# Optimization experiments

Measured on AMD Instinct MI355X. Metric: run time of the kernel, lower is better.

## Reference

```python
import jax, jax.numpy as jnp
import numpy as np

ROUTER_AUX_LOSS_COEF = 0.001


def setup_inputs() -> dict:
    key = jax.random.key(0)
    k1, k2, k3, k4 = jax.random.split(key, 4)
    B, S, H = 2, 2048, 2048
    E, I = 8, 768
    return {
        "hidden_states": jax.random.normal(k1, (B, S, H), dtype=jnp.float32),
        "gate_w": jax.random.normal(k2, (H, E), dtype=jnp.float32) * 0.02,
        "gate_up_proj": jax.random.normal(k3, (E, 2 * I, H), dtype=jnp.float32) * 0.02,
        "down_proj": jax.random.normal(k4, (E, H, I), dtype=jnp.float32) * 0.02,
        "num_experts_per_tok": 2,
    }


def reference(hidden_states, gate_w, gate_up_proj, down_proj, num_experts_per_tok):
    B, S, H = hidden_states.shape
    E = gate_w.shape[1]
    x = hidden_states.reshape(-1, H)  # (T, H)
    T = x.shape[0]

    # Router
    router_logits = x @ gate_w  # (T, E)
    routing_weights = jax.nn.softmax(router_logits, axis=-1)
    topk_w, selected = jax.lax.top_k(routing_weights, num_experts_per_tok)  # (T, K)
    topk_w = topk_w / jnp.sum(topk_w, axis=-1, keepdims=True)  # norm_topk_prob

    # Dense (T, E) combine weights: zero for non-selected experts. Identical math
    # to gathering per-token expert weights, but avoids materializing (T,K,2I,H).
    w_dense = jnp.zeros((T, E), x.dtype).at[jnp.arange(T)[:, None], selected].set(topk_w)

    # Expert GEMMs over all experts (non-selected contributions get weight 0)
    gate_up = jnp.einsum("th,efh->tef", x, gate_up_proj)  # (T, E, 2I)
    gate, up = jnp.split(gate_up, 2, axis=-1)
    inter = jax.nn.silu(gate) * up  # (T, E, I)
    expert_out = jnp.einsum("tei,ehi->teh", inter, down_proj)  # (T, E, H)
    final = jnp.einsum("teh,te->th", expert_out, w_dense).reshape(B, S, H)

    # Load-balancing auxiliary loss
    expert_probs = jnp.mean(routing_weights, axis=0)  # (E,)
    expert_mask = jax.nn.one_hot(selected, E, dtype=x.dtype)  # (T, K, E)
    expert_freq = jnp.mean(jnp.sum(expert_mask, axis=1), axis=0)  # (E,)
    aux_loss = jnp.sum(expert_probs * expert_freq) * E * ROUTER_AUX_LOSS_COEF

    return final, router_logits, aux_loss
```

## Files before the change

### kernel.cpp

```cpp
#include <hip/hip_runtime.h>
#include <hip/hip_bf16.h>
#include <math.h>

#define TT 4096
#define HH 2048
#define EE 8
#define II 768
#define TWOI 1536

typedef __attribute__((ext_vector_type(8))) short bf16v8;
typedef __attribute__((ext_vector_type(4))) float f32x4;

static __device__ __forceinline__ void cvt8f(const float4 v0, const float4 v1,
                                             uint4& hi, uint4& lo) {
    unsigned u[8] = {__float_as_uint(v0.x), __float_as_uint(v0.y),
                     __float_as_uint(v0.z), __float_as_uint(v0.w),
                     __float_as_uint(v1.x), __float_as_uint(v1.y),
                     __float_as_uint(v1.z), __float_as_uint(v1.w)};
    unsigned s[8];
#pragma unroll
    for (int i = 0; i < 8; ++i) {
        const float r = __uint_as_float(u[i]) - __uint_as_float(u[i] & 0xFFFF0000u);
        s[i] = __float_as_uint(r);
    }
    hi.x = __builtin_amdgcn_perm(u[1], u[0], 0x07060302);
    hi.y = __builtin_amdgcn_perm(u[3], u[2], 0x07060302);
    hi.z = __builtin_amdgcn_perm(u[5], u[4], 0x07060302);
    hi.w = __builtin_amdgcn_perm(u[7], u[6], 0x07060302);
    lo.x = __builtin_amdgcn_perm(s[1], s[0], 0x07060302);
    lo.y = __builtin_amdgcn_perm(s[3], s[2], 0x07060302);
    lo.z = __builtin_amdgcn_perm(s[5], s[4], 0x07060302);
    lo.w = __builtin_amdgcn_perm(s[7], s[6], 0x07060302);
}

__global__ __launch_bounds__(256) void router_kernel(
    const float* __restrict__ x, const float* __restrict__ gw,
    float* __restrict__ logits_out, int* __restrict__ counts,
    int* __restrict__ bucket_tok, float* __restrict__ bucket_w)
{
    const int wave = threadIdx.x >> 6;
    const int lane = threadIdx.x & 63;
    const int t = blockIdx.x * 4 + wave;

    float acc[EE];
#pragma unroll
    for (int e = 0; e < EE; ++e) acc[e] = 0.f;

    const float4* xr = (const float4*)(x + (size_t)t * HH);
    for (int i = lane; i < HH / 4; i += 64) {
        const float4 v = xr[i];
        const float* g = gw + (size_t)(i * 4) * EE;
#pragma unroll
        for (int e = 0; e < EE; ++e)
            acc[e] += v.x * g[e] + v.y * g[e + EE]
                    + v.z * g[e + 2 * EE] + v.w * g[e + 3 * EE];
    }
#pragma unroll
    for (int e = 0; e < EE; ++e) {
#pragma unroll
        for (int off = 32; off > 0; off >>= 1)
            acc[e] += __shfl_xor(acc[e], off, 64);
    }

    if (lane == 0) {
        float mx = acc[0];
#pragma unroll
        for (int e = 1; e < EE; ++e) mx = fmaxf(mx, acc[e]);
        float p[EE]; float s = 0.f;
#pragma unroll
        for (int e = 0; e < EE; ++e) { p[e] = expf(acc[e] - mx); s += p[e]; }
        const float inv = 1.f / s;
#pragma unroll
        for (int e = 0; e < EE; ++e) {
            p[e] *= inv;
            logits_out[(size_t)t * EE + e] = acc[e];
        }
        int i0 = 0;
#pragma unroll
        for (int e = 1; e < EE; ++e) if (p[e] > p[i0]) i0 = e;
        int i1 = (i0 == 0) ? 1 : 0;
#pragma unroll
        for (int e = 0; e < EE; ++e) if (e != i0 && p[e] > p[i1]) i1 = e;
        const float denom = 1.f / (p[i0] + p[i1]);
        const float w0 = p[i0] * denom, w1 = p[i1] * denom;
        int pos0 = atomicAdd(&counts[i0], 1);
        bucket_tok[i0 * TT + pos0] = t; bucket_w[i0 * TT + pos0] = w0;
        int pos1 = atomicAdd(&counts[i1], 1);
        bucket_tok[i1 * TT + pos1] = t; bucket_w[i1 * TT + pos1] = w1;
    }
}

__global__ __launch_bounds__(256) void finalize_router(
    const float* __restrict__ logits, const int* __restrict__ counts,
    int* __restrict__ offsets, float* __restrict__ aux_out)
{
    __shared__ float sums[EE];
    if (threadIdx.x < EE) sums[threadIdx.x] = 0.f;
    __syncthreads();
    float loc[EE];
#pragma unroll
    for (int e = 0; e < EE; ++e) loc[e] = 0.f;
    for (int t = threadIdx.x; t < TT; t += 256) {
        const float* lr = logits + (size_t)t * EE;
        float l[EE]; float mx = -1e30f;
#pragma unroll
        for (int e = 0; e < EE; ++e) { l[e] = lr[e]; mx = fmaxf(mx, l[e]); }
        float s = 0.f, p[EE];
#pragma unroll
        for (int e = 0; e < EE; ++e) { p[e] = expf(l[e] - mx); s += p[e]; }
        const float inv = 1.f / s;
#pragma unroll
        for (int e = 0; e < EE; ++e) loc[e] += p[e] * inv;
    }
#pragma unroll
    for (int e = 0; e < EE; ++e) atomicAdd(&sums[e], loc[e]);
    __syncthreads();
    if (threadIdx.x == 0) {
        int o = 0; float aux = 0.f;
        for (int e = 0; e < EE; ++e) {
            offsets[e] = o; o += counts[e];
            aux += (sums[e] / (float)TT) * ((float)counts[e] / (float)TT);
        }
        aux_out[0] = aux * (float)EE * 0.001f;
    }
}

#define AHI 0
#define ALO 10240
#define BHI 20480
#define BLO 30720
#define LROW 80

__global__ __launch_bounds__(256, 2) void moe_gateup_v3(
    const float* __restrict__ x, const float* __restrict__ Wgu,
    const int* __restrict__ counts, const int* __restrict__ offsets,
    const int* __restrict__ bucket_tok, float* __restrict__ inter)
{
    const int bid = blockIdx.x;
    const int e = bid & 7;
    const int rem = bid >> 3;
    const int mb = rem / 12, nb = rem % 12;

    const int cnt = counts[e];
    const int m0 = mb * 128;
    if (m0 >= cnt) return;
    const int n0 = nb * 64;
    const int base = offsets[e];

    __shared__ unsigned char smem[40960];

    const int tid = threadIdx.x;
    const int lane = tid & 63;
    const int wid = tid >> 6;
    const int wm = wid >> 1, wn = wid & 1;

    const int srow = tid >> 1;
    const int sseg = tid & 1;
    const int arow = m0 + srow;
    const int atok = (arow < cnt) ? bucket_tok[e * TT + arow] : 0;
    const float* ag = x + (size_t)atok * HH + sseg * 16;
    const int bblk = srow >> 5, bc = srow & 31;
    const int bj = ((bblk & 1) ? II : 0) + n0 + ((bblk >> 1) << 5) + bc;
    const float* bg = Wgu + ((size_t)e * TWOI + bj) * HH + sseg * 16;
    const int au0 = srow * LROW + (sseg * 2 + 0) * 16;
    const int au1 = srow * LROW + (sseg * 2 + 1) * 16;

    int aoff[4], boff[4];
#pragma unroll
    for (int i = 0; i < 4; ++i) {
        const int ra = wm * 64 + i * 16 + (lane & 15);
        aoff[i] = ra * LROW + (lane >> 4) * 16;
        const int rb = wn * 64 + i * 16 + (lane & 15);
        boff[i] = rb * LROW + (lane >> 4) * 16;
    }

    f32x4 acc[4][4];
#pragma unroll
    for (int i = 0; i < 4; ++i)
#pragma unroll
        for (int j = 0; j < 4; ++j) acc[i][j] = f32x4{0.f, 0.f, 0.f, 0.f};

    float4 pa0 = *(const float4*)(ag + 0), pa1 = *(const float4*)(ag + 4);
    float4 pa2 = *(const float4*)(ag + 8), pa3 = *(const float4*)(ag + 12);
    float4 pb0 = *(const float4*)(bg + 0), pb1 = *(const float4*)(bg + 4);
    float4 pb2 = *(const float4*)(bg + 8), pb3 = *(const float4*)(bg + 12);

    const int NS = HH / 32;
    for (int s = 0; s < NS; ++s) {
        __syncthreads();
        uint4 hi, lo;
        cvt8f(pa0, pa1, hi, lo);
        *(uint4*)(smem + AHI + au0) = hi; *(uint4*)(smem + ALO + au0) = lo;
        cvt8f(pa2, pa3, hi, lo);
        *(uint4*)(smem + AHI + au1) = hi; *(uint4*)(smem + ALO + au1) = lo;
        cvt8f(pb0, pb1, hi, lo);
        *(uint4*)(smem + BHI + au0) = hi; *(uint4*)(smem + BLO + au0) = lo;
        cvt8f(pb2, pb3, hi, lo);
        *(uint4*)(smem + BHI + au1) = hi; *(uint4*)(smem + BLO + au1) = lo;
        __syncthreads();
        if (s + 1 < NS) {
            const int k0 = (s + 1) * 32;
            pa0 = *(const float4*)(ag + k0); pa1 = *(const float4*)(ag + k0 + 4);
            pa2 = *(const float4*)(ag + k0 + 8); pa3 = *(const float4*)(ag + k0 + 12);
            pb0 = *(const float4*)(bg + k0); pb1 = *(const float4*)(bg + k0 + 4);
            pb2 = *(const float4*)(bg + k0 + 8); pb3 = *(const float4*)(bg + k0 + 12);
        }
        bf16v8 ah[4], al[4], bh[4], bl[4];
#pragma unroll
        for (int i = 0; i < 4; ++i) {
            ah[i] = *(const bf16v8*)(smem + AHI + aoff[i]);
            al[i] = *(const bf16v8*)(smem + ALO + aoff[i]);
            bh[i] = *(const bf16v8*)(smem + BHI + boff[i]);
            bl[i] = *(const bf16v8*)(smem + BLO + boff[i]);
        }
#pragma unroll
        for (int i = 0; i < 4; ++i)
#pragma unroll
            for (int j = 0; j < 4; ++j) {
                acc[i][j] = __builtin_amdgcn_mfma_f32_16x16x32_bf16(ah[i], bh[j], acc[i][j], 0, 0, 0);
                acc[i][j] = __builtin_amdgcn_mfma_f32_16x16x32_bf16(ah[i], bl[j], acc[i][j], 0, 0, 0);
                acc[i][j] = __builtin_amdgcn_mfma_f32_16x16x32_bf16(al[i], bh[j], acc[i][j], 0, 0, 0);
            }
    }

#pragma unroll
    for (int mi = 0; mi < 4; ++mi)
#pragma unroll
        for (int np = 0; np < 2; ++np) {
            const f32x4 g = acc[mi][np], u = acc[mi][np + 2];
            const int colp = n0 + wn * 32 + np * 16 + (lane & 15);
#pragma unroll
            for (int j = 0; j < 4; ++j) {
                const int r = m0 + wm * 64 + mi * 16 + ((lane >> 4) << 2) + j;
                if (r < cnt) {
                    const float gg = g[j];
                    const float sv = gg / (1.f + expf(-gg));
                    inter[(size_t)(base + r) * II + colp] = sv * u[j];
                }
            }
        }
}

__global__ __launch_bounds__(256, 2) void moe_down_v3(
    const float* __restrict__ inter, const float* __restrict__ Wd,
    const int* __restrict__ counts, const int* __restrict__ offsets,
    const int* __restrict__ bucket_tok, const float* __restrict__ bucket_w,
    float* __restrict__ out)
{
    const int bid = blockIdx.x;
    const int e = bid & 7;
    const int rem = bid >> 3;
    const int mb = rem >> 4, nb = rem & 15;

    const int cnt = counts[e];
    const int m0 = mb * 128;
    if (m0 >= cnt) return;
    const int n0 = nb * 128;
    const int base = offsets[e];

    __shared__ unsigned char smem[40960];

    const int tid = threadIdx.x;
    const int lane = tid & 63;
    const int wid = tid >> 6;
    const int wm = wid >> 1, wn = wid & 1;

    const int srow = tid >> 1;
    const int sseg = tid & 1;
    const int arow = m0 + srow;
    const int asafe = (arow < cnt) ? arow : 0;
    const float* ag = inter + (size_t)(base + asafe) * II + sseg * 16;
    const float* bg = Wd + ((size_t)e * HH + n0 + srow) * II + sseg * 16;
    const int au0 = srow * LROW + (sseg * 2 + 0) * 16;
    const int au1 = srow * LROW + (sseg * 2 + 1) * 16;

    int aoff[4], boff[4];
#pragma unroll
    for (int i = 0; i < 4; ++i) {
        const int ra = wm * 64 + i * 16 + (lane & 15);
        aoff[i] = ra * LROW + (lane >> 4) * 16;
        const int rb = wn * 64 + i * 16 + (lane & 15);
        boff[i] = rb * LROW + (lane >> 4) * 16;
    }

    f32x4 acc[4][4];
#pragma unroll
    for (int i = 0; i < 4; ++i)
#pragma unroll
        for (int j = 0; j < 4; ++j) acc[i][j] = f32x4{0.f, 0.f, 0.f, 0.f};

    float4 pa0 = *(const float4*)(ag + 0), pa1 = *(const float4*)(ag + 4);
    float4 pa2 = *(const float4*)(ag + 8), pa3 = *(const float4*)(ag + 12);
    float4 pb0 = *(const float4*)(bg + 0), pb1 = *(const float4*)(bg + 4);
    float4 pb2 = *(const float4*)(bg + 8), pb3 = *(const float4*)(bg + 12);

    const int NS = II / 32;
    for (int s = 0; s < NS; ++s) {
        __syncthreads();
        uint4 hi, lo;
        cvt8f(pa0, pa1, hi, lo);
        *(uint4*)(smem + AHI + au0) = hi; *(uint4*)(smem + ALO + au0) = lo;
        cvt8f(pa2, pa3, hi, lo);
        *(uint4*)(smem + AHI + au1) = hi; *(uint4*)(smem + ALO + au1) = lo;
        cvt8f(pb0, pb1, hi, lo);
        *(uint4*)(smem + BHI + au0) = hi; *(uint4*)(smem + BLO + au0) = lo;
        cvt8f(pb2, pb3, hi, lo);
        *(uint4*)(smem + BHI + au1) = hi; *(uint4*)(smem + BLO + au1) = lo;
        __syncthreads();
        if (s + 1 < NS) {
            const int k0 = (s + 1) * 32;
            pa0 = *(const float4*)(ag + k0); pa1 = *(const float4*)(ag + k0 + 4);
            pa2 = *(const float4*)(ag + k0 + 8); pa3 = *(const float4*)(ag + k0 + 12);
            pb0 = *(const float4*)(bg + k0); pb1 = *(const float4*)(bg + k0 + 4);
            pb2 = *(const float4*)(bg + k0 + 8); pb3 = *(const float4*)(bg + k0 + 12);
        }
        bf16v8 ah[4], al[4], bh[4], bl[4];
#pragma unroll
        for (int i = 0; i < 4; ++i) {
            ah[i] = *(const bf16v8*)(smem + AHI + aoff[i]);
            al[i] = *(const bf16v8*)(smem + ALO + aoff[i]);
            bh[i] = *(const bf16v8*)(smem + BHI + boff[i]);
            bl[i] = *(const bf16v8*)(smem + BLO + boff[i]);
        }
#pragma unroll
        for (int i = 0; i < 4; ++i)
#pragma unroll
            for (int j = 0; j < 4; ++j) {
                acc[i][j] = __builtin_amdgcn_mfma_f32_16x16x32_bf16(ah[i], bh[j], acc[i][j], 0, 0, 0);
                acc[i][j] = __builtin_amdgcn_mfma_f32_16x16x32_bf16(ah[i], bl[j], acc[i][j], 0, 0, 0);
                acc[i][j] = __builtin_amdgcn_mfma_f32_16x16x32_bf16(al[i], bh[j], acc[i][j], 0, 0, 0);
            }
    }

#pragma unroll
    for (int mi = 0; mi < 4; ++mi) {
        int rtok[4]; float rw[4]; int rok[4];
#pragma unroll
        for (int j = 0; j < 4; ++j) {
            const int r = m0 + wm * 64 + mi * 16 + ((lane >> 4) << 2) + j;
            rok[j] = (r < cnt);
            rtok[j] = rok[j] ? bucket_tok[e * TT + r] : 0;
            rw[j] = rok[j] ? bucket_w[e * TT + r] : 0.f;
        }
#pragma unroll
        for (int ni = 0; ni < 4; ++ni) {
            const int col = n0 + wn * 64 + ni * 16 + (lane & 15);
#pragma unroll
            for (int j = 0; j < 4; ++j)
                if (rok[j])
                    atomicAdd(out + (size_t)rtok[j] * HH + col, rw[j] * acc[mi][ni][j]);
        }
    }
}

extern "C" void kernel_launch(void* const* d_in, const int* in_sizes, int n_in,
                              void* d_out, int out_size, void* d_ws, size_t ws_size,
                              hipStream_t stream)
{
    const float* x   = (const float*)d_in[0];
    const float* gw  = (const float*)d_in[1];
    const float* wgu = (const float*)d_in[2];
    const float* wd  = (const float*)d_in[3];

    float* out_final  = (float*)d_out;
    float* out_logits = out_final + (size_t)TT * HH;
    float* out_aux    = out_logits + (size_t)TT * EE;

    int*   counts     = (int*)d_ws;
    int*   offsets    = counts + 8;
    int*   bucket_tok = (int*)d_ws + 64;
    float* bucket_w   = (float*)d_ws + 64 + EE * TT;
    float* inter      = (float*)d_ws + 64 + 2 * EE * TT;

    hipMemsetAsync(d_ws, 0, 256, stream);
    hipMemsetAsync(d_out, 0, sizeof(float) * (size_t)TT * HH, stream);

    router_kernel<<<TT / 4, 256, 0, stream>>>(x, gw, out_logits, counts,
                                              bucket_tok, bucket_w);
    finalize_router<<<1, 256, 0, stream>>>(out_logits, counts, offsets, out_aux);
    moe_gateup_v3<<<12 * 32 * EE, 256, 0, stream>>>(x, wgu, counts, offsets,
                                                    bucket_tok, inter);
    moe_down_v3<<<16 * 32 * EE, 256, 0, stream>>>(inter, wd, counts, offsets,
                                                  bucket_tok, bucket_w, out_final);
}
```

Before: 647.5 us.

## Enlarge expert GEMM tiles to 128x256 with per-wave full-M layout

Both expert GEMM kernels switch from 128x128 tiles on a 2x2 wave grid to wider tiles (N doubled). Each wave now covers all 128 rows and a 64-column slice, so B fragments stay in registers and A fragments are streamed from shared memory. The goal is to cut global loads and the fp32-to-bf16 split conversion of A per FLOP, and to halve the block count. The cost is a larger shared memory footprint (60KB) and doubled accumulator registers (128 floats), which may lower occupancy or cause spills under launch_bounds(256,2).

```diff
diff --git a/kernel.cpp b/kernel.cpp
--- a/kernel.cpp
+++ b/kernel.cpp
@@ -128,10 +128,10 @@
 #define AHI 0
 #define ALO 10240
 #define BHI 20480
-#define BLO 30720
+#define BLO 40960
 #define LROW 80
 
-__global__ __launch_bounds__(256, 2) void moe_gateup_v3(
+__global__ __launch_bounds__(256, 2) void moe_gateup_v4(
     const float* __restrict__ x, const float* __restrict__ Wgu,
     const int* __restrict__ counts, const int* __restrict__ offsets,
     const int* __restrict__ bucket_tok, float* __restrict__ inter)
@@ -139,51 +139,67 @@
     const int bid = blockIdx.x;
     const int e = bid & 7;
     const int rem = bid >> 3;
-    const int mb = rem / 12, nb = rem % 12;
+    const int mb = rem / 6, nb = rem % 6;
 
     const int cnt = counts[e];
     const int m0 = mb * 128;
     if (m0 >= cnt) return;
-    const int n0 = nb * 64;
+    const int n0 = nb * 128;
     const int base = offsets[e];
 
-    __shared__ unsigned char smem[40960];
+    __shared__ unsigned char smem[61440];
 
     const int tid = threadIdx.x;
     const int lane = tid & 63;
-    const int wid = tid >> 6;
-    const int wm = wid >> 1, wn = wid & 1;
+    const int w = tid >> 6;
 
     const int srow = tid >> 1;
     const int sseg = tid & 1;
     const int arow = m0 + srow;
     const int atok = (arow < cnt) ? bucket_tok[e * TT + arow] : 0;
     const float* ag = x + (size_t)atok * HH + sseg * 16;
-    const int bblk = srow >> 5, bc = srow & 31;
-    const int bj = ((bblk & 1) ? II : 0) + n0 + ((bblk >> 1) << 5) + bc;
-    const float* bg = Wgu + ((size_t)e * TWOI + bj) * HH + sseg * 16;
+
+    int bcol[2];
+#pragma unroll
+    for (int h = 0; h < 2; ++h) {
+        const int r = srow + h * 128;
+        const int wq = r >> 6, sub = r & 63;
+        bcol[h] = ((sub >> 5) ? II : 0) + n0 + wq * 32 + (sub & 31);
+    }
+    const float* bg0 = Wgu + ((size_t)e * TWOI + bcol[0]) * HH + sseg * 16;
+    const float* bg1 = Wgu + ((size_t)e * TWOI + bcol[1]) * HH + sseg * 16;
+
     const int au0 = srow * LROW + (sseg * 2 + 0) * 16;
     const int au1 = srow * LROW + (sseg * 2 + 1) * 16;
-
-    int aoff[4], boff[4];
-#pragma unroll
-    for (int i = 0; i < 4; ++i) {
-        const int ra = wm * 64 + i * 16 + (lane & 15);
+    const int bu0 = srow * LROW + (sseg * 2 + 0) * 16;
+    const int bu1 = srow * LROW + (sseg * 2 + 1) * 16;
+    const int bv0 = (srow + 128) * LROW + (sseg * 2 + 0) * 16;
+    const int bv1 = (srow + 128) * LROW + (sseg * 2 + 1) * 16;
+
+    int aoff[8], boff[4];
+#pragma unroll
+    for (int i = 0; i < 8; ++i) {
+        const int ra = i * 16 + (lane & 15);
         aoff[i] = ra * LROW + (lane >> 4) * 16;
-        const int rb = wn * 64 + i * 16 + (lane & 15);
-        boff[i] = rb * LROW + (lane >> 4) * 16;
-    }
-
-    f32x4 acc[4][4];
-#pragma unroll
-    for (int i = 0; i < 4; ++i)
+    }
+#pragma unroll
+    for (int j = 0; j < 4; ++j) {
+        const int rb = w * 64 + j * 16 + (lane & 15);
+        boff[j] = rb * LROW + (lane >> 4) * 16;
+    }
+
+    f32x4 acc[8][4];
+#pragma unroll
+    for (int i = 0; i < 8; ++i)
 #pragma unroll
         for (int j = 0; j < 4; ++j) acc[i][j] = f32x4{0.f, 0.f, 0.f, 0.f};
 
     float4 pa0 = *(const float4*)(ag + 0), pa1 = *(const float4*)(ag + 4);
     float4 pa2 = *(const float4*)(ag + 8), pa3 = *(const float4*)(ag + 12);
-    float4 pb0 = *(const float4*)(bg + 0), pb1 = *(const float4*)(bg + 4);
-    float4 pb2 = *(const float4*)(bg + 8), pb3 = *(const float4*)(bg + 12);
+    float4 pb0 = *(const float4*)(bg0 + 0), pb1 = *(const float4*)(bg0 + 4);
+    float4 pb2 = *(const float4*)(bg0 + 8), pb3 = *(const float4*)(bg0 + 12);
+    float4 pc0 = *(const float4*)(bg1 + 0), pc1 = *(const float4*)(bg1 + 4);
+    float4 pc2 = *(const float4*)(bg1 + 8), pc3 = *(const float4*)(bg1 + 12);
 
     const int NS = HH / 32;
     for (int s = 0; s < NS; ++s) {
@@ -194,44 +210,51 @@
         cvt8f(pa2, pa3, hi, lo);
         *(uint4*)(smem + AHI + au1) = hi; *(uint4*)(smem + ALO + au1) = lo;
         cvt8f(pb0, pb1, hi, lo);
-        *(uint4*)(smem + BHI + au0) = hi; *(uint4*)(smem + BLO + au0) = lo;
+        *(uint4*)(smem + BHI + bu0) = hi; *(uint4*)(smem + BLO + bu0) = lo;
         cvt8f(pb2, pb3, hi, lo);
-        *(uint4*)(smem + BHI + au1) = hi; *(uint4*)(smem + BLO + au1) = lo;
+        *(uint4*)(smem + BHI + bu1) = hi; *(uint4*)(smem + BLO + bu1) = lo;
+        cvt8f(pc0, pc1, hi, lo);
+        *(uint4*)(smem + BHI + bv0) = hi; *(uint4*)(smem + BLO + bv0) = lo;
+        cvt8f(pc2, pc3, hi, lo);
+        *(uint4*)(smem + BHI + bv1) = hi; *(uint4*)(smem + BLO + bv1) = lo;
         __syncthreads();
         if (s + 1 < NS) {
             const int k0 = (s + 1) * 32;
             pa0 = *(const float4*)(ag + k0); pa1 = *(const float4*)(ag + k0 + 4);
             pa2 = *(const float4*)(ag + k0 + 8); pa3 = *(const float4*)(ag + k0 + 12);
-            pb0 = *(const float4*)(bg + k0); pb1 = *(const float4*)(bg + k0 + 4);
-            pb2 = *(const float4*)(bg + k0 + 8); pb3 = *(const float4*)(bg + k0 + 12);
-        }
-        bf16v8 ah[4], al[4], bh[4], bl[4];
-#pragma unroll
-        for (int i = 0; i < 4; ++i) {
-            ah[i] = *(const bf16v8*)(smem + AHI + aoff[i]);
-            al[i] = *(const bf16v8*)(smem + ALO + aoff[i]);
-            bh[i] = *(const bf16v8*)(smem + BHI + boff[i]);
-            bl[i] = *(const bf16v8*)(smem + BLO + boff[i]);
-        }
-#pragma unroll
-        for (int i = 0; i < 4; ++i)
+            pb0 = *(const float4*)(bg0 + k0); pb1 = *(const float4*)(bg0 + k0 + 4);
+            pb2 = *(const float4*)(bg0 + k0 + 8); pb3 = *(const float4*)(bg0 + k0 + 12);
+            pc0 = *(const float4*)(bg1 + k0); pc1 = *(const float4*)(bg1 + k0 + 4);
+            pc2 = *(const float4*)(bg1 + k0 + 8); pc3 = *(const float4*)(bg1 + k0 + 12);
+        }
+        bf16v8 bh[4], bl[4];
+#pragma unroll
+        for (int j = 0; j < 4; ++j) {
+            bh[j] = *(const bf16v8*)(smem + BHI + boff[j]);
+            bl[j] = *(const bf16v8*)(smem + BLO + boff[j]);
+        }
+#pragma unroll
+        for (int i = 0; i < 8; ++i) {
+            const bf16v8 ah = *(const bf16v8*)(smem + AHI + aoff[i]);
+            const bf16v8 al = *(const bf16v8*)(smem + ALO + aoff[i]);
 #pragma unroll
             for (int j = 0; j < 4; ++j) {
-                acc[i][j] = __builtin_amdgcn_mfma_f32_16x16x32_bf16(ah[i], bh[j], acc[i][j], 0, 0, 0);
-                acc[i][j] = __builtin_amdgcn_mfma_f32_16x16x32_bf16(ah[i], bl[j], acc[i][j], 0, 0, 0);
-                acc[i][j] = __builtin_amdgcn_mfma_f32_16x16x32_bf16(al[i], bh[j], acc[i][j], 0, 0, 0);
+                acc[i][j] = __builtin_amdgcn_mfma_f32_16x16x32_bf16(ah, bh[j], acc[i][j], 0, 0, 0);
+                acc[i][j] = __builtin_amdgcn_mfma_f32_16x16x32_bf16(ah, bl[j], acc[i][j], 0, 0, 0);
+                acc[i][j] = __builtin_amdgcn_mfma_f32_16x16x32_bf16(al, bh[j], acc[i][j], 0, 0, 0);
             }
-    }
-
-#pragma unroll
-    for (int mi = 0; mi < 4; ++mi)
+        }
+    }
+
+#pragma unroll
+    for (int mi = 0; mi < 8; ++mi)
 #pragma unroll
         for (int np = 0; np < 2; ++np) {
             const f32x4 g = acc[mi][np], u = acc[mi][np + 2];
-            const int colp = n0 + wn * 32 + np * 16 + (lane & 15);
+            const int colp = n0 + w * 32 + np * 16 + (lane & 15);
 #pragma unroll
             for (int j = 0; j < 4; ++j) {
-                const int r = m0 + wm * 64 + mi * 16 + ((lane >> 4) << 2) + j;
+                const int r = m0 + mi * 16 + ((lane >> 4) << 2) + j;
                 if (r < cnt) {
                     const float gg = g[j];
                     const float sv = gg / (1.f + expf(-gg));
@@ -241,7 +264,7 @@
         }
 }
 
-__global__ __launch_bounds__(256, 2) void moe_down_v3(
+__global__ __launch_bounds__(256, 2) void moe_down_v4(
     const float* __restrict__ inter, const float* __restrict__ Wd,
     const int* __restrict__ counts, const int* __restrict__ offsets,
     const int* __restrict__ bucket_tok, const float* __restrict__ bucket_w,
@@ -250,49 +273,58 @@
     const int bid = blockIdx.x;
     const int e = bid & 7;
     const int rem = bid >> 3;
-    const int mb = rem >> 4, nb = rem & 15;
+    const int mb = rem >> 3, nb = rem & 7;
 
     const int cnt = counts[e];
     const int m0 = mb * 128;
     if (m0 >= cnt) return;
-    const int n0 = nb * 128;
+    const int n0 = nb * 256;
     const int base = offsets[e];
 
-    __shared__ unsigned char smem[40960];
+    __shared__ unsigned char smem[61440];
 
     const int tid = threadIdx.x;
     const int lane = tid & 63;
-    const int wid = tid >> 6;
-    const int wm = wid >> 1, wn = wid & 1;
+    const int w = tid >> 6;
 
     const int srow = tid >> 1;
     const int sseg = tid & 1;
     const int arow = m0 + srow;
     const int asafe = (arow < cnt) ? arow : 0;
     const float* ag = inter + (size_t)(base + asafe) * II + sseg * 16;
-    const float* bg = Wd + ((size_t)e * HH + n0 + srow) * II + sseg * 16;
+    const float* bg0 = Wd + ((size_t)e * HH + n0 + srow) * II + sseg * 16;
+    const float* bg1 = Wd + ((size_t)e * HH + n0 + srow + 128) * II + sseg * 16;
+
     const int au0 = srow * LROW + (sseg * 2 + 0) * 16;
     const int au1 = srow * LROW + (sseg * 2 + 1) * 16;
-
-    int aoff[4], boff[4];
-#pragma unroll
-    for (int i = 0; i < 4; ++i) {
-        const int ra = wm * 64 + i * 16 + (lane & 15);
+    const int bu0 = au0, bu1 = au1;
+    const int bv0 = (srow + 128) * LROW + (sseg * 2 + 0) * 16;
+    const int bv1 = (srow + 128) * LROW + (sseg * 2 + 1) * 16;
+
+    int aoff[8], boff[4];
+#pragma unroll
+    for (int i = 0; i < 8; ++i) {
+        const int ra = i * 16 + (lane & 15);
         aoff[i] = ra * LROW + (lane >> 4) * 16;
-        const int rb = wn * 64 + i * 16 + (lane & 15);
-        boff[i] = rb * LROW + (lane >> 4) * 16;
-    }
-
-    f32x4 acc[4][4];
-#pragma unroll
-    for (int i = 0; i < 4; ++i)
+    }
+#pragma unroll
+    for (int j = 0; j < 4; ++j) {
+        const int rb = w * 64 + j * 16 + (lane & 15);
+        boff[j] = rb * LROW + (lane >> 4) * 16;
+    }
+
+    f32x4 acc[8][4];
+#pragma unroll
+    for (int i = 0; i < 8; ++i)
 #pragma unroll
         for (int j = 0; j < 4; ++j) acc[i][j] = f32x4{0.f, 0.f, 0.f, 0.f};
 
     float4 pa0 = *(const float4*)(ag + 0), pa1 = *(const float4*)(ag + 4);
     float4 pa2 = *(const float4*)(ag + 8), pa3 = *(const float4*)(ag + 12);
-    float4 pb0 = *(const float4*)(bg + 0), pb1 = *(const float4*)(bg + 4);
-    float4 pb2 = *(const float4*)(bg + 8), pb3 = *(const float4*)(bg + 12);
+    float4 pb0 = *(const float4*)(bg0 + 0), pb1 = *(const float4*)(bg0 + 4);
+    float4 pb2 = *(const float4*)(bg0 + 8), pb3 = *(const float4*)(bg0 + 12);
+    float4 pc0 = *(const float4*)(bg1 + 0), pc1 = *(const float4*)(bg1 + 4);
+    float4 pc2 = *(const float4*)(bg1 + 8), pc3 = *(const float4*)(bg1 + 12);
 
     const int NS = II / 32;
     for (int s = 0; s < NS; ++s) {
@@ -303,48 +335,55 @@
         cvt8f(pa2, pa3, hi, lo);
         *(uint4*)(smem + AHI + au1) = hi; *(uint4*)(smem + ALO + au1) = lo;
         cvt8f(pb0, pb1, hi, lo);
-        *(uint4*)(smem + BHI + au0) = hi; *(uint4*)(smem + BLO + au0) = lo;
+        *(uint4*)(smem + BHI + bu0) = hi; *(uint4*)(smem + BLO + bu0) = lo;
         cvt8f(pb2, pb3, hi, lo);
-        *(uint4*)(smem + BHI + au1) = hi; *(uint4*)(smem + BLO + au1) = lo;
+        *(uint4*)(smem + BHI + bu1) = hi; *(uint4*)(smem + BLO + bu1) = lo;
+        cvt8f(pc0, pc1, hi, lo);
+        *(uint4*)(smem + BHI + bv0) = hi; *(uint4*)(smem + BLO + bv0) = lo;
+        cvt8f(pc2, pc3, hi, lo);
+        *(uint4*)(smem + BHI + bv1) = hi; *(uint4*)(smem + BLO + bv1) = lo;
         __syncthreads();
         if (s + 1 < NS) {
             const int k0 = (s + 1) * 32;
             pa0 = *(const float4*)(ag + k0); pa1 = *(const float4*)(ag + k0 + 4);
             pa2 = *(const float4*)(ag + k0 + 8); pa3 = *(const float4*)(ag + k0 + 12);
-            pb0 = *(const float4*)(bg + k0); pb1 = *(const float4*)(bg + k0 + 4);
-            pb2 = *(const float4*)(bg + k0 + 8); pb3 = *(const float4*)(bg + k0 + 12);
-        }
-        bf16v8 ah[4], al[4], bh[4], bl[4];
-#pragma unroll
-        for (int i = 0; i < 4; ++i) {
-            ah[i] = *(const bf16v8*)(smem + AHI + aoff[i]);
-            al[i] = *(const bf16v8*)(smem + ALO + aoff[i]);
-            bh[i] = *(const bf16v8*)(smem + BHI + boff[i]);
-            bl[i] = *(const bf16v8*)(smem + BLO + boff[i]);
-        }
-#pragma unroll
-        for (int i = 0; i < 4; ++i)
+            pb0 = *(const float4*)(bg0 + k0); pb1 = *(const float4*)(bg0 + k0 + 4);
+            pb2 = *(const float4*)(bg0 + k0 + 8); pb3 = *(const float4*)(bg0 + k0 + 12);
+            pc0 = *(const float4*)(bg1 + k0); pc1 = *(const float4*)(bg1 + k0 + 4);
+            pc2 = *(const float4*)(bg1 + k0 + 8); pc3 = *(const float4*)(bg1 + k0 + 12);
+        }
+        bf16v8 bh[4], bl[4];
+#pragma unroll
+        for (int j = 0; j < 4; ++j) {
+            bh[j] = *(const bf16v8*)(smem + BHI + boff[j]);
+            bl[j] = *(const bf16v8*)(smem + BLO + boff[j]);
+        }
+#pragma unroll
+        for (int i = 0; i < 8; ++i) {
+            const bf16v8 ah = *(const bf16v8*)(smem + AHI + aoff[i]);
+            const bf16v8 al = *(const bf16v8*)(smem + ALO + aoff[i]);
 #pragma unroll
             for (int j = 0; j < 4; ++j) {
-                acc[i][j] = __builtin_amdgcn_mfma_f32_16x16x32_bf16(ah[i], bh[j], acc[i][j], 0, 0, 0);
-                acc[i][j] = __builtin_amdgcn_mfma_f32_16x16x32_bf16(ah[i], bl[j], acc[i][j], 0, 0, 0);
-                acc[i][j] = __builtin_amdgcn_mfma_f32_16x16x32_bf16(al[i], bh[j], acc[i][j], 0, 0, 0);
+                acc[i][j] = __builtin_amdgcn_mfma_f32_16x16x32_bf16(ah, bh[j], acc[i][j], 0, 0, 0);
+                acc[i][j] = __builtin_amdgcn_mfma_f32_16x16x32_bf16(ah, bl[j], acc[i][j], 0, 0, 0);
+                acc[i][j] = __builtin_amdgcn_mfma_f32_16x16x32_bf16(al, bh[j], acc[i][j], 0, 0, 0);
             }
-    }
-
-#pragma unroll
-    for (int mi = 0; mi < 4; ++mi) {
+        }
+    }
+
+#pragma unroll
+    for (int mi = 0; mi < 8; ++mi) {
         int rtok[4]; float rw[4]; int rok[4];
 #pragma unroll
         for (int j = 0; j < 4; ++j) {
-            const int r = m0 + wm * 64 + mi * 16 + ((lane >> 4) << 2) + j;
+            const int r = m0 + mi * 16 + ((lane >> 4) << 2) + j;
             rok[j] = (r < cnt);
             rtok[j] = rok[j] ? bucket_tok[e * TT + r] : 0;
             rw[j] = rok[j] ? bucket_w[e * TT + r] : 0.f;
         }
 #pragma unroll
         for (int ni = 0; ni < 4; ++ni) {
-            const int col = n0 + wn * 64 + ni * 16 + (lane & 15);
+            const int col = n0 + w * 64 + ni * 16 + (lane & 15);
 #pragma unroll
             for (int j = 0; j < 4; ++j)
                 if (rok[j])
@@ -378,8 +417,8 @@
     router_kernel<<<TT / 4, 256, 0, stream>>>(x, gw, out_logits, counts,
                                               bucket_tok, bucket_w);
     finalize_router<<<1, 256, 0, stream>>>(out_logits, counts, offsets, out_aux);
-    moe_gateup_v3<<<12 * 32 * EE, 256, 0, stream>>>(x, wgu, counts, offsets,
-                                                    bucket_tok, inter);
-    moe_down_v3<<<16 * 32 * EE, 256, 0, stream>>>(inter, wd, counts, offsets,
-                                                  bucket_tok, bucket_w, out_final);
-}
+    moe_gateup_v4<<<6 * 32 * EE, 256, 0, stream>>>(x, wgu, counts, offsets,
+                                                   bucket_tok, inter);
+    moe_down_v4<<<8 * 32 * EE, 256, 0, stream>>>(inter, wd, counts, offsets,
+                                                 bucket_tok, bucket_w, out_final);
+}
```

Result: faster. 632.4 us (-2.3%).
